# Kernel tuning notes

Measured on AMD Instinct MI355X. Metric: run time of the kernel, lower is better.

## Reference

```python
import jax, jax.numpy as jnp
import numpy as np

NUM_CLASSES = 100
ALPHA = 2.0
EPS = 1e-12  # torch F.normalize eps


def setup_inputs() -> dict:
    key = jax.random.key(0)
    k1, k2, k3 = jax.random.split(key, 3)
    B, D, C = 16384, 1024, NUM_CLASSES
    x = jax.random.normal(k1, (B, D), dtype=jnp.float32)
    W = jax.random.normal(k2, (D, C), dtype=jnp.float32) * 0.02  # linear classifier head: px = x @ W
    y = jax.random.randint(k3, (B,), 0, C)
    return {"x": x, "W": W, "y": y}


def _norm_cos(a, b):
    # dot(F.normalize(a), F.normalize(b)) per row, eps-clamped norms like torch
    an = a / jnp.maximum(jnp.linalg.norm(a, axis=-1, keepdims=True), EPS)
    bn = b / jnp.maximum(jnp.linalg.norm(b, axis=-1, keepdims=True), EPS)
    return jnp.sum(an * bn, axis=-1)


def reference(x, W, y):
    C = NUM_CLASSES
    # px = x @ W ; per-sample cross entropy
    logits = x @ W                                    # [B, C]
    logp = jax.nn.log_softmax(logits, axis=-1)
    ce = -jnp.take_along_axis(logp, y[:, None], axis=1)[:, 0]   # [B]
    # closed-form d(sum ce)/dx = (softmax - onehot) @ W^T  (create_graph analogue: still a fn of x, W)
    onehot = jax.nn.one_hot(y, C, dtype=x.dtype)
    grad_x = (jnp.exp(logp) - onehot) @ W.T           # [B, D]

    # per-class segment reductions (strategy='all')
    class_sum = jax.ops.segment_sum(grad_x, y, num_segments=C)          # [C, D]
    counts = jax.ops.segment_sum(jnp.ones_like(ce), y, num_segments=C)  # [C]
    total = jnp.sum(grad_x, axis=0)                                     # [D]

    # anchor = argmin CE within each class
    mask = (y[None, :] == jnp.arange(C)[:, None])     # [C, B]
    masked_ce = jnp.where(mask, ce[None, :], jnp.inf)
    anchor_idx = jnp.argmin(masked_ce, axis=1)        # [C]
    grad_a = grad_x[anchor_idx]                       # [C, D]

    # grad_p = sum over positives excluding anchor (zero when class has 1 sample)
    grad_p = class_sum - grad_a
    # grad_n = sum over negatives
    grad_n = total[None, :] - class_sum

    term = _norm_cos(grad_a, grad_p) - _norm_cos(grad_a, grad_n)  # [C]
    present = counts > 0
    n_present = jnp.maximum(jnp.sum(present), 1).astype(ce.dtype)
    triplet = jnp.sum(jnp.where(present, term, 0.0)) / n_present

    loss = jnp.mean(ce - ALPHA * triplet)
    return loss
```

## Files before the change

### kernel.cpp

```cpp
#include <hip/hip_runtime.h>
#include <stdint.h>

#define BN 16384
#define DK 1024
#define CN 100
#define CP 112
#define CP2 224
#define THREADS 256
#define KS 32
#define NSTEP (DK / KS)
#define KSPLIT 4
#define WK (DK / KSPLIT)
#define WSTEP (WK / KS)
#define STEPE (CP2 * KS)
#define GP 112
#define PSB 64
#define PSR (BN / PSB)

typedef __attribute__((ext_vector_type(4))) float f32x4;
typedef __attribute__((ext_vector_type(8))) short bf16x8;
typedef unsigned short ushort_t;
typedef unsigned int uint_t;

__device__ __forceinline__ ushort_t f2bf(float f) {
    uint_t u = __float_as_uint(f);
    uint_t r = u + 0x7FFFu + ((u >> 16) & 1u);
    return (ushort_t)(r >> 16);
}
__device__ __forceinline__ float bf2f(ushort_t h) {
    return __uint_as_float(((uint_t)h) << 16);
}
__device__ __forceinline__ float getf(const float4& v, int e) {
    return e == 0 ? v.x : e == 1 ? v.y : e == 2 ? v.z : v.w;
}

__global__ __launch_bounds__(256) void k_prep(const float* __restrict__ W,
        ushort_t* __restrict__ wB, unsigned long long* __restrict__ packed,
        int* __restrict__ counts, float* ce_sum, float* term_sum, int* present) {
    __shared__ float tile[8][CN];
    const int tid = threadIdx.x;
    const int b = blockIdx.x;
    const int st = b >> 2, kq8 = (b & 3) * 8;
    const float* src = W + (size_t)(st * KS + kq8) * CN;
    for (int i = tid; i < 8 * CN; i += 256) {
        int kk = i / CN;
        tile[kk][i - kk * CN] = src[i];
    }
    __syncthreads();
    for (int j = tid; j < CP * 8; j += 256) {
        int c = j >> 3, kk = j & 7;
        float v = (c < CN) ? tile[kk][c] : 0.f;
        ushort_t hb = f2bf(v);
        ushort_t lb = f2bf(v - bf2f(hb));
        size_t o = (size_t)st * STEPE + (size_t)c * KS + kq8 + kk;
        wB[o] = hb;
        wB[o + (size_t)CP * KS] = lb;
    }
    if (b == 0) {
        if (tid < CN) { packed[tid] = ~0ULL; counts[tid] = 0; }
        if (tid == 0) { *ce_sum = 0.f; *term_sum = 0.f; *present = 0; }
    }
}

__global__ __launch_bounds__(THREADS) void k_main(
    const float* __restrict__ x, const ushort_t* __restrict__ wB,
    const int* __restrict__ y, ushort_t* __restrict__ g_buf,
    unsigned long long* __restrict__ packed, int* __restrict__ counts,
    float* __restrict__ ce_sum) {

    __shared__ float cacc[KSPLIT][64][29];

    const int tid = threadIdx.x;
    const int lane = tid & 63;
    const int wv = tid >> 6;
    const int l15 = lane & 15;
    const int lg = lane >> 4;
    const int row0 = blockIdx.x * 16;

    const float* xg = x + (size_t)(row0 + l15) * DK + wv * WK + lg * 8;
    const ushort_t* wg = wB + (size_t)(wv * WSTEP) * STEPE + (size_t)l15 * KS + lg * 8;

    f32x4 acc[7];
#pragma unroll
    for (int t = 0; t < 7; ++t) acc[t] = (f32x4){0.f, 0.f, 0.f, 0.f};

#pragma unroll
    for (int s = 0; s < WSTEP; ++s) {
        float4 xa = *(const float4*)(xg + s * KS);
        float4 xb = *(const float4*)(xg + s * KS + 4);
        bf16x8 ah, al;
#pragma unroll
        for (int e = 0; e < 4; ++e) {
            float f0 = getf(xa, e);
            float f1 = getf(xb, e);
            ushort_t h0 = f2bf(f0), h1 = f2bf(f1);
            ushort_t l0 = f2bf(f0 - bf2f(h0)), l1 = f2bf(f1 - bf2f(h1));
            ah[e] = (short)h0; ah[e + 4] = (short)h1;
            al[e] = (short)l0; al[e + 4] = (short)l1;
        }
        const ushort_t* bp = wg + (size_t)s * STEPE;
#pragma unroll
        for (int t = 0; t < 7; ++t) {
            bf16x8 bh = *(const bf16x8*)(bp + t * (16 * KS));
            acc[t] = __builtin_amdgcn_mfma_f32_16x16x32_bf16(ah, bh, acc[t], 0, 0, 0);
            acc[t] = __builtin_amdgcn_mfma_f32_16x16x32_bf16(al, bh, acc[t], 0, 0, 0);
        }
    }

#pragma unroll
    for (int t = 0; t < 7; ++t)
#pragma unroll
        for (int e = 0; e < 4; ++e) cacc[wv][lane][t * 4 + e] = acc[t][e];
    __syncthreads();
    if (wv != 0) return;
#pragma unroll
    for (int t = 0; t < 7; ++t)
#pragma unroll
        for (int e = 0; e < 4; ++e)
            acc[t][e] = cacc[0][lane][t * 4 + e] + cacc[1][lane][t * 4 + e] +
                        cacc[2][lane][t * 4 + e] + cacc[3][lane][t * 4 + e];

    float ce_acc = 0.f;
#pragma unroll
    for (int rr = 0; rr < 4; ++rr) {
        const int grow = row0 + lg * 4 + rr;
        const int yr = y[grow];
        float m = -3.4e38f;
#pragma unroll
        for (int t = 0; t < 7; ++t) {
            int c = l15 + 16 * t;
            if (c < CN) m = fmaxf(m, acc[t][rr]);
        }
#pragma unroll
        for (int s = 1; s < 16; s <<= 1) m = fmaxf(m, __shfl_xor(m, s));
        float ev[7], ssum = 0.f;
#pragma unroll
        for (int t = 0; t < 7; ++t) {
            int c = l15 + 16 * t;
            ev[t] = (c < CN) ? __expf(acc[t][rr] - m) : 0.f;
            ssum += ev[t];
        }
#pragma unroll
        for (int s = 1; s < 16; s <<= 1) ssum += __shfl_xor(ssum, s);
        const float lse = m + __logf(ssum);
        const float inv = 1.f / ssum;
#pragma unroll
        for (int t = 0; t < 7; ++t) {
            int c = l15 + 16 * t;
            float g = (c < CN) ? (ev[t] * inv - ((c == yr) ? 1.f : 0.f)) : 0.f;
            g_buf[(size_t)grow * GP + c] = f2bf(g);
            if (c == yr) {
                float ce = lse - acc[t][rr];
                ce_acc += ce;
                unsigned long long pk =
                    ((unsigned long long)__float_as_uint(fmaxf(ce, 0.f)) << 32) |
                    (unsigned int)grow;
                atomicMin(&packed[yr], pk);
                atomicAdd(&counts[yr], 1);
            }
        }
    }
#pragma unroll
    for (int s = 1; s < 64; s <<= 1) ce_acc += __shfl_xor(ce_acc, s);
    if (lane == 0) atomicAdd(ce_sum, ce_acc);
}

__global__ __launch_bounds__(256) void k_gram(const ushort_t* __restrict__ wB,
                                              float* __restrict__ M) {
    __shared__ float gacc[4][64][4];
    const int tid = threadIdx.x;
    const int lane = tid & 63, wvv = tid >> 6;
    const int c1t = blockIdx.x / 7, c2t = blockIdx.x % 7;
    const int l15 = lane & 15, lg = lane >> 4;
    const ushort_t* pa = wB + (size_t)(c1t * 16 + l15) * KS + lg * 8;
    const ushort_t* pb = wB + (size_t)(c2t * 16 + l15) * KS + lg * 8;
    f32x4 acc = (f32x4){0.f, 0.f, 0.f, 0.f};
#pragma unroll
    for (int i = 0; i < 8; ++i) {
        const size_t o = (size_t)(wvv * 8 + i) * STEPE;
        bf16x8 ah = *(const bf16x8*)(pa + o);
        bf16x8 al = *(const bf16x8*)(pa + o + CP * KS);
        bf16x8 bh = *(const bf16x8*)(pb + o);
        bf16x8 bl = *(const bf16x8*)(pb + o + CP * KS);
        acc = __builtin_amdgcn_mfma_f32_16x16x32_bf16(ah, bh, acc, 0, 0, 0);
        acc = __builtin_amdgcn_mfma_f32_16x16x32_bf16(ah, bl, acc, 0, 0, 0);
        acc = __builtin_amdgcn_mfma_f32_16x16x32_bf16(al, bh, acc, 0, 0, 0);
    }
#pragma unroll
    for (int e = 0; e < 4; ++e) gacc[wvv][lane][e] = acc[e];
    __syncthreads();
    if (tid < 64) {
#pragma unroll
        for (int e = 0; e < 4; ++e) {
            float s = gacc[0][tid][e] + gacc[1][tid][e] + gacc[2][tid][e] + gacc[3][tid][e];
            int row = (tid >> 4) * 4 + e, col = tid & 15;
            M[(size_t)(c1t * 16 + row) * CP + c2t * 16 + col] = s;
        }
    }
}

__global__ __launch_bounds__(256) void k_psum(const int* __restrict__ y,
        const ushort_t* __restrict__ g_buf, float* __restrict__ partial) {
    __shared__ float acc[2][CN][CP];
    const int tid = threadIdx.x;
    const int team = tid >> 7, j = tid & 127;
    float* af = (float*)acc;
    for (int i = tid; i < 2 * CN * CP; i += 256) af[i] = 0.f;
    __syncthreads();
    const int rbase = blockIdx.x * PSR + team;
    for (int ch = 0; ch < PSR / 2; ch += 8) {
        ushort_t v[8];
        int cl[8];
#pragma unroll
        for (int q = 0; q < 8; ++q) {
            const int row = rbase + (ch + q) * 2;
            cl[q] = y[row];
            v[q] = (j < CP) ? g_buf[(size_t)row * GP + j] : (ushort_t)0;
        }
#pragma unroll
        for (int q = 0; q < 8; ++q)
            if (j < CP) acc[team][cl[q]][j] += bf2f(v[q]);
    }
    __syncthreads();
    float* out = partial + (size_t)blockIdx.x * (CN * CP);
    for (int i = tid; i < CN * CP; i += 256) out[i] = af[i] + af[i + CN * CP];
}

__global__ __launch_bounds__(256) void k_reduce(const float* __restrict__ partial,
                                                float* __restrict__ cls) {
    const int i = blockIdx.x * 256 + threadIdx.x;
    if (i >= CN * CP) return;
    float s = 0.f;
#pragma unroll 8
    for (int b = 0; b < PSB; ++b) s += partial[(size_t)b * (CN * CP) + i];
    cls[i] = s;
}

__global__ __launch_bounds__(128) void k_class(
    const float* __restrict__ M, const ushort_t* __restrict__ g_buf,
    const float* __restrict__ cls, const int* __restrict__ counts,
    const unsigned long long* __restrict__ packed,
    float* __restrict__ term_sum, int* __restrict__ present) {
    __shared__ float a_s[CP], p_s[CP], n_s[CP];
    __shared__ float wsum[2][5];
    const int c = blockIdx.x, t = threadIdx.x;
    if (counts[c] == 0) return;
    const int anchor = (int)(packed[c] & 0xffffffffULL);
    if (t < CP) {
        float a = bf2f(g_buf[(size_t)anchor * GP + t]);
        float cs = cls[c * CP + t];
        float tot = 0.f;
#pragma unroll 8
        for (int k = 0; k < CN; ++k) tot += cls[k * CP + t];
        a_s[t] = a; p_s[t] = cs - a; n_s[t] = tot - cs;
    }
    __syncthreads();
    float aa = 0, ap = 0, pp = 0, an = 0, nn = 0;
    if (t < CP) {
        float ua = 0, up = 0, un = 0;
#pragma unroll 8
        for (int k = 0; k < CP; ++k) {
            float m = M[(size_t)k * CP + t];
            ua = fmaf(m, a_s[k], ua);
            up = fmaf(m, p_s[k], up);
            un = fmaf(m, n_s[k], un);
        }
        aa = a_s[t] * ua; ap = a_s[t] * up; pp = p_s[t] * up;
        an = a_s[t] * un; nn = n_s[t] * un;
    }
#pragma unroll
    for (int s = 1; s < 64; s <<= 1) {
        aa += __shfl_xor(aa, s); ap += __shfl_xor(ap, s); pp += __shfl_xor(pp, s);
        an += __shfl_xor(an, s); nn += __shfl_xor(nn, s);
    }
    const int wid = t >> 6;
    if ((t & 63) == 0) {
        wsum[wid][0] = aa; wsum[wid][1] = ap; wsum[wid][2] = pp;
        wsum[wid][3] = an; wsum[wid][4] = nn;
    }
    __syncthreads();
    if (t == 0) {
        aa = wsum[0][0] + wsum[1][0];
        ap = wsum[0][1] + wsum[1][1];
        pp = wsum[0][2] + wsum[1][2];
        an = wsum[0][3] + wsum[1][3];
        nn = wsum[0][4] + wsum[1][4];
        float na  = sqrtf(fmaxf(aa, 0.f));
        float np_ = sqrtf(fmaxf(pp, 0.f));
        float nn_ = sqrtf(fmaxf(nn, 0.f));
        float cos_ap = ap / (fmaxf(na, 1e-12f) * fmaxf(np_, 1e-12f));
        float cos_an = an / (fmaxf(na, 1e-12f) * fmaxf(nn_, 1e-12f));
        atomicAdd(term_sum, cos_ap - cos_an);
        atomicAdd(present, 1);
    }
}

__global__ void k_final(const float* ce_sum, const float* term_sum,
                        const int* present, float* out) {
    float npres = fmaxf((float)(*present), 1.f);
    out[0] = (*ce_sum) * (1.f / (float)BN) - 2.0f * ((*term_sum) / npres);
}

extern "C" void kernel_launch(void* const* d_in, const int* in_sizes, int n_in,
                              void* d_out, int out_size, void* d_ws, size_t ws_size,
                              hipStream_t stream) {
    const float* x = (const float*)d_in[0];
    const float* W = (const float*)d_in[1];
    const int* y = (const int*)d_in[2];

    char* ws = (char*)d_ws;
    ushort_t* wB      = (ushort_t*)(ws);
    ushort_t* g_buf   = (ushort_t*)(ws + 458752);
    float*    partial = (float*)(ws + 4128768);
    float*    cls     = (float*)(ws + 6995968);
    float*    M       = (float*)(ws + 7040768);
    unsigned long long* packed = (unsigned long long*)(ws + 7090944);
    int*      counts  = (int*)(ws + 7091744);
    float*    ce_sum  = (float*)(ws + 7092144);
    float*    term_sum= (float*)(ws + 7092148);
    int*      present = (int*)(ws + 7092152);

    k_prep<<<128, 256, 0, stream>>>(W, wB, packed, counts, ce_sum, term_sum, present);
    k_main<<<BN / 16, THREADS, 0, stream>>>(x, wB, y, g_buf, packed, counts, ce_sum);
    k_gram<<<49, 256, 0, stream>>>(wB, M);
    k_psum<<<PSB, 256, 0, stream>>>(y, g_buf, partial);
    k_reduce<<<(CN * CP + 255) / 256, 256, 0, stream>>>(partial, cls);
    k_class<<<CN, 128, 0, stream>>>(M, g_buf, cls, counts, packed, term_sum, present);
    k_final<<<1, 1, 0, stream>>>(ce_sum, term_sum, present, (float*)d_out);
}
```

Measured before the change: 181.9 us.

## Spread softmax epilogue across all waves and move anchor atomics to dedicated kernel

After the split-K reduction in k_main, each of the four waves now handles one row of the 16-row tile's softmax and gradient epilogue, where previously only wave 0 did all four. Per-sample CE is written to a new buffer instead of being accumulated with global atomicMin/atomicAdd on per-class slots. A new single-block k_anchor kernel reads that buffer and computes the per-class argmin, counts and CE sum using shared-memory atomics. This removes contended global atomics and the idle waves from the main kernel, at the cost of an extra launch and a serial pass over 16K samples in one block.

```diff
diff --git a/kernel.cpp b/kernel.cpp
--- a/kernel.cpp
+++ b/kernel.cpp
@@ -35,8 +35,7 @@
 }
 
 __global__ __launch_bounds__(256) void k_prep(const float* __restrict__ W,
-        ushort_t* __restrict__ wB, unsigned long long* __restrict__ packed,
-        int* __restrict__ counts, float* ce_sum, float* term_sum, int* present) {
+        ushort_t* __restrict__ wB, float* term_sum, int* present) {
     __shared__ float tile[8][CN];
     const int tid = threadIdx.x;
     const int b = blockIdx.x;
@@ -56,17 +55,13 @@
         wB[o] = hb;
         wB[o + (size_t)CP * KS] = lb;
     }
-    if (b == 0) {
-        if (tid < CN) { packed[tid] = ~0ULL; counts[tid] = 0; }
-        if (tid == 0) { *ce_sum = 0.f; *term_sum = 0.f; *present = 0; }
-    }
+    if (b == 0 && tid == 0) { *term_sum = 0.f; *present = 0; }
 }
 
 __global__ __launch_bounds__(THREADS) void k_main(
     const float* __restrict__ x, const ushort_t* __restrict__ wB,
     const int* __restrict__ y, ushort_t* __restrict__ g_buf,
-    unsigned long long* __restrict__ packed, int* __restrict__ counts,
-    float* __restrict__ ce_sum) {
+    float* __restrict__ ce_buf) {
 
     __shared__ float cacc[KSPLIT][64][29];
 
@@ -112,57 +107,75 @@
 #pragma unroll
         for (int e = 0; e < 4; ++e) cacc[wv][lane][t * 4 + e] = acc[t][e];
     __syncthreads();
-    if (wv != 0) return;
+
+    float pv[7];
 #pragma unroll
     for (int t = 0; t < 7; ++t)
-#pragma unroll
-        for (int e = 0; e < 4; ++e)
-            acc[t][e] = cacc[0][lane][t * 4 + e] + cacc[1][lane][t * 4 + e] +
-                        cacc[2][lane][t * 4 + e] + cacc[3][lane][t * 4 + e];
-
-    float ce_acc = 0.f;
-#pragma unroll
-    for (int rr = 0; rr < 4; ++rr) {
-        const int grow = row0 + lg * 4 + rr;
-        const int yr = y[grow];
-        float m = -3.4e38f;
-#pragma unroll
-        for (int t = 0; t < 7; ++t) {
-            int c = l15 + 16 * t;
-            if (c < CN) m = fmaxf(m, acc[t][rr]);
-        }
-#pragma unroll
-        for (int s = 1; s < 16; s <<= 1) m = fmaxf(m, __shfl_xor(m, s));
-        float ev[7], ssum = 0.f;
-#pragma unroll
-        for (int t = 0; t < 7; ++t) {
-            int c = l15 + 16 * t;
-            ev[t] = (c < CN) ? __expf(acc[t][rr] - m) : 0.f;
-            ssum += ev[t];
-        }
-#pragma unroll
-        for (int s = 1; s < 16; s <<= 1) ssum += __shfl_xor(ssum, s);
-        const float lse = m + __logf(ssum);
-        const float inv = 1.f / ssum;
-#pragma unroll
-        for (int t = 0; t < 7; ++t) {
-            int c = l15 + 16 * t;
-            float g = (c < CN) ? (ev[t] * inv - ((c == yr) ? 1.f : 0.f)) : 0.f;
-            g_buf[(size_t)grow * GP + c] = f2bf(g);
-            if (c == yr) {
-                float ce = lse - acc[t][rr];
-                ce_acc += ce;
-                unsigned long long pk =
-                    ((unsigned long long)__float_as_uint(fmaxf(ce, 0.f)) << 32) |
-                    (unsigned int)grow;
-                atomicMin(&packed[yr], pk);
-                atomicAdd(&counts[yr], 1);
-            }
-        }
-    }
-#pragma unroll
-    for (int s = 1; s < 64; s <<= 1) ce_acc += __shfl_xor(ce_acc, s);
-    if (lane == 0) atomicAdd(ce_sum, ce_acc);
+        pv[t] = cacc[0][lane][t * 4 + wv] + cacc[1][lane][t * 4 + wv] +
+                cacc[2][lane][t * 4 + wv] + cacc[3][lane][t * 4 + wv];
+
+    const int grow = row0 + lg * 4 + wv;
+    const int yr = y[grow];
+    float m = -3.4e38f;
+#pragma unroll
+    for (int t = 0; t < 7; ++t) {
+        int c = l15 + 16 * t;
+        if (c < CN) m = fmaxf(m, pv[t]);
+    }
+#pragma unroll
+    for (int s = 1; s < 16; s <<= 1) m = fmaxf(m, __shfl_xor(m, s));
+    float ev[7], ssum = 0.f;
+#pragma unroll
+    for (int t = 0; t < 7; ++t) {
+        int c = l15 + 16 * t;
+        ev[t] = (c < CN) ? __expf(pv[t] - m) : 0.f;
+        ssum += ev[t];
+    }
+#pragma unroll
+    for (int s = 1; s < 16; s <<= 1) ssum += __shfl_xor(ssum, s);
+    const float lse = m + __logf(ssum);
+    const float inv = 1.f / ssum;
+#pragma unroll
+    for (int t = 0; t < 7; ++t) {
+        int c = l15 + 16 * t;
+        float g = (c < CN) ? (ev[t] * inv - ((c == yr) ? 1.f : 0.f)) : 0.f;
+        g_buf[(size_t)grow * GP + c] = f2bf(g);
+        if (c == yr) ce_buf[grow] = lse - pv[t];
+    }
+}
+
+__global__ __launch_bounds__(1024) void k_anchor(const int* __restrict__ y,
+        const float* __restrict__ ce_buf, unsigned long long* __restrict__ packed,
+        int* __restrict__ counts, float* __restrict__ ce_sum) {
+    __shared__ unsigned long long lp[CN];
+    __shared__ int lc[CN];
+    __shared__ float lsum[16];
+    const int tid = threadIdx.x;
+    if (tid < CN) { lp[tid] = ~0ULL; lc[tid] = 0; }
+    __syncthreads();
+    float se = 0.f;
+#pragma unroll
+    for (int it = 0; it < BN / 1024; ++it) {
+        const int i = tid + it * 1024;
+        const int yr = y[i];
+        const float ce = ce_buf[i];
+        se += ce;
+        unsigned long long pk =
+            ((unsigned long long)__float_as_uint(fmaxf(ce, 0.f)) << 32) | (unsigned int)i;
+        atomicMin(&lp[yr], pk);
+        atomicAdd(&lc[yr], 1);
+    }
+#pragma unroll
+    for (int s = 1; s < 64; s <<= 1) se += __shfl_xor(se, s);
+    if ((tid & 63) == 0) lsum[tid >> 6] = se;
+    __syncthreads();
+    if (tid < CN) { packed[tid] = lp[tid]; counts[tid] = lc[tid]; }
+    if (tid == 0) {
+        float t = 0.f;
+#pragma unroll
+        for (int w = 0; w < 16; ++w) t += lsum[w];
+        *ce_sum = t;
+    }
 }
 
 __global__ __launch_bounds__(256) void k_gram(const ushort_t* __restrict__ wB,
@@ -316,14 +329,16 @@
     float*    M       = (float*)(ws + 7040768);
     unsigned long long* packed = (unsigned long long*)(ws + 7090944);
     int*      counts  = (int*)(ws + 7091744);
-    float*    ce_sum  = (float*)(ws + 7092144);
-    float*    term_sum= (float*)(ws + 7092148);
-    int*      present = (int*)(ws + 7092152);
-
-    k_prep<<<128, 256, 0, stream>>>(W, wB, packed, counts, ce_sum, term_sum, present);
-    k_main<<<BN / 16, THREADS, 0, stream>>>(x, wB, y, g_buf, packed, counts, ce_sum);
+    float*    ce_buf  = (float*)(ws + 7092160);
+    float*    ce_sum  = (float*)(ws + 7157696);
+    float*    term_sum= (float*)(ws + 7157700);
+    int*      present = (int*)(ws + 7157704);
+
+    k_prep<<<128, 256, 0, stream>>>(W, wB, term_sum, present);
+    k_main<<<BN / 16, THREADS, 0, stream>>>(x, wB, y, g_buf, ce_buf);
     k_gram<<<49, 256, 0, stream>>>(wB, M);
     k_psum<<<PSB, 256, 0, stream>>>(y, g_buf, partial);
+    k_anchor<<<1, 1024, 0, stream>>>(y, ce_buf, packed, counts, ce_sum);
     k_reduce<<<(CN * CP + 255) / 256, 256, 0, stream>>>(partial, cls);
     k_class<<<CN, 128, 0, stream>>>(M, g_buf, cls, counts, packed, term_sum, present);
     k_final<<<1, 1, 0, stream>>>(ce_sum, term_sum, present, (float*)d_out);
```

New measurement: 158.8 us. 12.7% less time.
